# Optimization experiments

Measured on AMD Instinct MI355X. Metric: run time of the kernel, lower is better.

Reference implementation:

```python
import jax, jax.numpy as jnp
import numpy as np

B = 1024          # batch of positions
K = 64            # king squares
F = 640           # 64 squares * 10 piece types
C = 256           # accumulator channels


def setup_inputs() -> dict:
    key = jax.random.key(0)
    k1, k2, k3 = jax.random.split(key, 3)
    piece_positions = jax.random.randint(k1, (B, 64, 10), 0, 2).astype(jnp.bool_)
    king_positions = jax.random.randint(k2, (B, 2), 0, K, dtype=jnp.int32)
    input_weights = jax.random.normal(k3, (K, F + 1, C), dtype=jnp.float32)
    bias = jnp.zeros((C,), dtype=jnp.float32)
    return {
        "piece_positions": piece_positions,
        "king_positions": king_positions,
        "input_weights": input_weights,
        "bias": bias,
    }


def reference(piece_positions, king_positions, input_weights, bias):
    # Flatten the (64, 10) boolean piece plane into 640 HalfKP features.
    b = piece_positions.shape[0]
    p = piece_positions.reshape(b, F).astype(input_weights.dtype)          # (B, 640)
    # Gather each sample's white/black king weight slabs: (B, 2, 641, 256)
    Wg = jnp.take(input_weights, king_positions, axis=0)
    # Sparse-feature sum for both halves, contracted over feature dim and
    # summed over the two king perspectives in one einsum.
    halves = jnp.einsum("bf,bsfc->bc", p, Wg[:, :, :F, :])                 # (B, 256)
    extra = Wg[:, :, F, :].sum(axis=1)                                     # row 640 for each king
    return halves + extra + bias
```

## Files before the change

### kernel.cpp

```cpp
#include <hip/hip_runtime.h>
#include <hip/hip_bf16.h>


#define F_DIM 640
#define C_DIM 256
#define SLAB_STRIDE (641 * 256)
#define NKING 64
#define NBAND 7
#define WROWS 96
#define WPR 48
#define WSTR 260
#define LCAP 256
#define NC_MAX 64

#define WS_MASK_OFF 0
#define WS_PART_OFF 81920
#define WS_NEED (WS_PART_OFF + NBAND * 2 * 1024 * 256 * 4)

typedef float  f32x4  __attribute__((ext_vector_type(4)));
typedef short  bf16x8 __attribute__((ext_vector_type(8)));

__device__ __forceinline__ unsigned f2bf_pk(float a, float b) {
    union { float f; unsigned u; } x, y;
    x.f = a; y.f = b;
    const unsigned ra = (x.u + 0x7FFFu + ((x.u >> 16) & 1u)) >> 16;
    const unsigned rb = (y.u + 0x7FFFu + ((y.u >> 16) & 1u)) >> 16;
    return (ra & 0xFFFFu) | (rb << 16);
}

__device__ __forceinline__ bf16x8 mk_a8(unsigned m32, int g) {
    const unsigned by = (m32 >> (g * 8)) & 0xFFu;
    union { unsigned u[4]; bf16x8 v; } r;
    #pragma unroll
    for (int i = 0; i < 4; ++i)
        r.u[i] = (((by >> (2 * i)) & 1u) ? 0x3F80u : 0u) |
                 (((by >> (2 * i + 1)) & 1u) ? 0x3F800000u : 0u);
    return r.v;
}

__global__ __launch_bounds__(256)
void pack_masks(const int* __restrict__ pieces,
                unsigned long long* __restrict__ mask,
                int nwords)
{
    const int gw = blockIdx.x * 4 + (threadIdx.x >> 6);
    const int lane = threadIdx.x & 63;
    if (gw >= nwords) return;
    const int v = pieces[(size_t)gw * 64 + lane];
    const unsigned long long m = __ballot(v != 0);
    if (lane == 0) mask[gw] = m;
}

__global__ __launch_bounds__(512, 4)
void halfkp_kband(const float* __restrict__ W,
                  const unsigned long long* __restrict__ mask,
                  const int* __restrict__ kings,
                  float* __restrict__ partial,
                  int nent)
{
    const int k  = blockIdx.x;
    const int bd = blockIdx.y;
    const int t  = threadIdx.x;
    const int wv = t >> 6, lane = t & 63;
    const int mt = wv & 1;
    const int cg = wv >> 1;
    const int li = lane & 15, g = lane >> 4;

    __shared__ unsigned s_W[WPR * WSTR];
    __shared__ int s_ent[LCAP];
    __shared__ int s_cb[NC_MAX + 1];
    __shared__ unsigned s_m32[64][3];
    __shared__ int s_nk;

    const int r0 = bd * WROWS;
    const float* __restrict__ Wk = W + (size_t)k * SLAB_STRIDE;
    float4 ve[6], vo[6];
    #pragma unroll
    for (int it = 0; it < 6; ++it) {
        const int task = t + (it << 9);
        const int pr = task >> 6, c4 = task & 63;
        const int fe = min(r0 + 2 * pr, F_DIM);
        const int fo = min(r0 + 2 * pr + 1, F_DIM);
        ve[it] = *(const float4*)&Wk[(size_t)fe * C_DIM + c4 * 4];
        vo[it] = *(const float4*)&Wk[(size_t)fo * C_DIM + c4 * 4];
    }

    {
        const int NC = nent >> 6;
        const int nit = NC >> 3;
        unsigned long long mm[8];
        #pragma unroll
        for (int it = 0; it < 8; ++it) {
            if (it < nit) {
                const int c = wv + (it << 3);
                const int kk = kings[(c << 6) + lane];
                mm[it] = __ballot(kk == k);
                if (lane == 0) s_cb[c] = (int)__popcll(mm[it]);
            }
        }
        __syncthreads();
        if (t == 0) {
            int s = 0;
            for (int c = 0; c < NC; ++c) { const int v = s_cb[c]; s_cb[c] = s; s += v; }
            s_nk = min(s, LCAP);
        }
        __syncthreads();
        const unsigned long long lt = (1ull << lane) - 1ull;
        #pragma unroll
        for (int it = 0; it < 8; ++it) {
            if (it < nit) {
                const int c = wv + (it << 3);
                if ((mm[it] >> lane) & 1ull) {
                    const int pos = s_cb[c] + (int)__popcll(mm[it] & lt);
                    if (pos < LCAP) s_ent[pos] = (c << 6) + lane;
                }
            }
        }
    }
    __syncthreads();
    const int n_k = s_nk;

    {
        const int ncc0 = min(n_k, 64);
        for (int idx = t; idx < 64 * 3; idx += 512) {
            const int row = idx & 63, ksl = idx >> 6;
            const int ksg = bd * 3 + ksl;
            const int id = (row < ncc0) ? s_ent[row] : -1;
            unsigned v = 0;
            if (id >= 0) {
                if (ksg < 20) {
                    const unsigned long long mw = mask[(size_t)(id >> 1) * 10 + (ksg >> 1)];
                    v = (unsigned)(mw >> ((ksg & 1) * 32));
                } else {
                    v = 1u;
                }
            }
            s_m32[row][ksl] = v;
        }
    }

    #pragma unroll
    for (int it = 0; it < 6; ++it) {
        const int task = t + (it << 9);
        const int pr = task >> 6, c4 = task & 63;
        union { unsigned u[4]; f32x4 v; } pk;
        pk.u[0] = f2bf_pk(ve[it].x, vo[it].x);
        pk.u[1] = f2bf_pk(ve[it].y, vo[it].y);
        pk.u[2] = f2bf_pk(ve[it].z, vo[it].z);
        pk.u[3] = f2bf_pk(ve[it].w, vo[it].w);
        *(f32x4*)&s_W[pr * WSTR + c4 * 4] = pk.v;
    }
    __syncthreads();

    for (int mb = 0; mb < n_k; mb += 64) {
        const int ncc = min(n_k - mb, 64);

        if (mb > 0) {
            __syncthreads();
            for (int idx = t; idx < 64 * 3; idx += 512) {
                const int row = idx & 63, ksl = idx >> 6;
                const int ksg = bd * 3 + ksl;
                const int id = (row < ncc) ? s_ent[mb + row] : -1;
                unsigned v = 0;
                if (id >= 0) {
                    if (ksg < 20) {
                        const unsigned long long mw = mask[(size_t)(id >> 1) * 10 + (ksg >> 1)];
                        v = (unsigned)(mw >> ((ksg & 1) * 32));
                    } else {
                        v = 1u;
                    }
                }
                s_m32[row][ksl] = v;
            }
            __syncthreads();
        }

        #pragma unroll
        for (int tb = 0; tb < 4; tb += 2) {
            const int tile = tb + mt;
            if (tile * 16 < ncc) {
                f32x4 acc[4];
                #pragma unroll
                for (int nt = 0; nt < 4; ++nt) acc[nt] = (f32x4){0.f, 0.f, 0.f, 0.f};
                const unsigned* mrow = s_m32[tile * 16 + li];
                #pragma unroll
                for (int ksl = 0; ksl < 3; ++ksl) {
                    const bf16x8 af = mk_a8(mrow[ksl], g);
                    #pragma unroll
                    for (int nt = 0; nt < 4; ++nt) {
                        const unsigned* bp =
                            &s_W[(ksl * 16 + g * 4) * WSTR + cg * 64 + nt * 16 + li];
                        union { unsigned u[4]; bf16x8 v; } bb;
                        bb.u[0] = bp[0];
                        bb.u[1] = bp[WSTR];
                        bb.u[2] = bp[2 * WSTR];
                        bb.u[3] = bp[3 * WSTR];
                        acc[nt] = __builtin_amdgcn_mfma_f32_16x16x32_bf16(af, bb.v, acc[nt], 0, 0, 0);
                    }
                }
                #pragma unroll
                for (int i = 0; i < 4; ++i) {
                    const int r = tile * 16 + 4 * g + i;
                    if (r < ncc) {
                        const int id = s_ent[mb + r];
                        float* dst = &partial[(((size_t)(bd * 2 + (id & 1))) * 1024
                                              + (id >> 1)) * C_DIM + cg * 64];
                        #pragma unroll
                        for (int nt = 0; nt < 4; ++nt)
                            dst[nt * 16 + li] = acc[nt][i];
                    }
                }
            }
        }
    }
}

__global__ __launch_bounds__(256)
void finalize(const float* __restrict__ partial,
              const float* __restrict__ bias,
              float* __restrict__ out)
{
    const int i = blockIdx.x * 256 + threadIdx.x;
    float4 s = ((const float4*)bias)[i & 63];
    #pragma unroll
    for (int sl = 0; sl < NBAND * 2; ++sl) {
        const float4 p = ((const float4*)partial)[(size_t)sl * 1024 * 64 + i];
        s.x += p.x; s.y += p.y; s.z += p.z; s.w += p.w;
    }
    ((float4*)out)[i] = s;
}

__global__ __launch_bounds__(256)
void halfkp_fallback(const int* __restrict__ pieces, const int* __restrict__ kings,
                     const float* __restrict__ W, const float* __restrict__ bias,
                     float* __restrict__ out)
{
    const int b = blockIdx.x;
    const int c = threadIdx.x;
    const int lane = c & 63;
    const int k0 = kings[2 * b + 0];
    const int k1 = kings[2 * b + 1];
    const float* W0 = W + (size_t)k0 * SLAB_STRIDE + c;
    const float* W1 = W + (size_t)k1 * SLAB_STRIDE + c;
    float acc = bias[c] + W0[640 * 256] + W1[640 * 256];
    const int* pi = pieces + (size_t)b * F_DIM;
    #pragma unroll
    for (int ch = 0; ch < 10; ++ch) {
        int v = pi[ch * 64 + lane];
        unsigned long long m = __ballot(v != 0);
        const float* b0 = W0 + ch * 64 * 256;
        const float* b1 = W1 + ch * 64 * 256;
        while (m) {
            const int f = __builtin_ctzll(m);
            m &= m - 1;
            acc += b0[f * 256] + b1[f * 256];
        }
    }
    out[(size_t)b * C_DIM + c] = acc;
}

extern "C" void kernel_launch(void* const* d_in, const int* in_sizes, int n_in,
                              void* d_out, int out_size, void* d_ws, size_t ws_size,
                              hipStream_t stream) {
    const int* pieces = (const int*)d_in[0];
    const int* kings  = (const int*)d_in[1];
    const float* W    = (const float*)d_in[2];
    const float* bias = (const float*)d_in[3];
    float* out        = (float*)d_out;

    const int B = in_sizes[1] / 2;
    const int nent = 2 * B;
    const int nwords = B * 10;

    if (ws_size < (size_t)WS_NEED) {
        halfkp_fallback<<<dim3(B), dim3(C_DIM), 0, stream>>>(pieces, kings, W, bias, out);
        return;
    }

    unsigned long long* mask = (unsigned long long*)((char*)d_ws + WS_MASK_OFF);
    float* part = (float*)((char*)d_ws + WS_PART_OFF);

    pack_masks<<<dim3((nwords + 3) / 4), dim3(256), 0, stream>>>(pieces, mask, nwords);
    halfkp_kband<<<dim3(NKING, NBAND), dim3(512), 0, stream>>>(W, mask, kings, part, nent);
    finalize<<<dim3(B * 64 / 256), dim3(256), 0, stream>>>(part, bias, out);
}
```

Baseline: 27.87 us.

## Stage fp32 weight slabs via direct global-to-LDS loads with per-chunk bf16 conversion

Replaces the register-staged weight load, which converted to packed bf16 before writing LDS, with global_load_lds DMA of raw fp32 rows into a swizzled 32-row LDS buffer. The 96-row band is processed in three 32-row chunks, with a sync and restage between each, and bf16 packing is done at read time with v_cvt_pk_bf16_f32. This removes the register round-trip and shrinks LDS use, which could raise occupancy. The cost is extra barriers and serialised load-compute per chunk, plus conversion work repeated for every tile. For later mb iterations the weights are reloaded because the chunk buffer is overwritten.

```diff
diff --git a/kernel.cpp b/kernel.cpp
--- a/kernel.cpp
+++ b/kernel.cpp
@@ -7,9 +7,6 @@
 #define SLAB_STRIDE (641 * 256)
 #define NKING 64
 #define NBAND 7
-#define WROWS 96
-#define WPR 48
-#define WSTR 260
 #define LCAP 256
 #define NC_MAX 64
 
@@ -20,12 +17,10 @@
 typedef float  f32x4  __attribute__((ext_vector_type(4)));
 typedef short  bf16x8 __attribute__((ext_vector_type(8)));
 
-__device__ __forceinline__ unsigned f2bf_pk(float a, float b) {
-    union { float f; unsigned u; } x, y;
-    x.f = a; y.f = b;
-    const unsigned ra = (x.u + 0x7FFFu + ((x.u >> 16) & 1u)) >> 16;
-    const unsigned rb = (y.u + 0x7FFFu + ((y.u >> 16) & 1u)) >> 16;
-    return (ra & 0xFFFFu) | (rb << 16);
+__device__ __forceinline__ void gl_lds16(const float* g, unsigned* l) {
+    __builtin_amdgcn_global_load_lds(
+        (const __attribute__((address_space(1))) void*)g,
+        (__attribute__((address_space(3))) void*)l, 16, 0, 0);
 }
 
 __device__ __forceinline__ bf16x8 mk_a8(unsigned m32, int g) {
@@ -52,11 +47,11 @@
 }
 
 __global__ __launch_bounds__(512, 4)
-void halfkp_kband(const float* __restrict__ W,
-                  const unsigned long long* __restrict__ mask,
-                  const int* __restrict__ kings,
-                  float* __restrict__ partial,
-                  int nent)
+void halfkp_dma(const float* __restrict__ W,
+                const unsigned long long* __restrict__ mask,
+                const int* __restrict__ kings,
+                float* __restrict__ partial,
+                int nent)
 {
     const int k  = blockIdx.x;
     const int bd = blockIdx.y;
@@ -66,24 +61,27 @@
     const int cg = wv >> 1;
     const int li = lane & 15, g = lane >> 4;
 
-    __shared__ unsigned s_W[WPR * WSTR];
+    __shared__ unsigned s_Wf[32 * 256];
     __shared__ int s_ent[LCAP];
     __shared__ int s_cb[NC_MAX + 1];
     __shared__ unsigned s_m32[64][3];
     __shared__ int s_nk;
 
-    const int r0 = bd * WROWS;
     const float* __restrict__ Wk = W + (size_t)k * SLAB_STRIDE;
-    float4 ve[6], vo[6];
-    #pragma unroll
-    for (int it = 0; it < 6; ++it) {
-        const int task = t + (it << 9);
-        const int pr = task >> 6, c4 = task & 63;
-        const int fe = min(r0 + 2 * pr, F_DIM);
-        const int fo = min(r0 + 2 * pr + 1, F_DIM);
-        ve[it] = *(const float4*)&Wk[(size_t)fe * C_DIM + c4 * 4];
-        vo[it] = *(const float4*)&Wk[(size_t)fo * C_DIM + c4 * 4];
-    }
+
+    #define STAGE(ws_)                                                        \
+        {                                                                     \
+            _Pragma("unroll")                                                 \
+            for (int q = 0; q < 4; ++q) {                                     \
+                const int wr = wv * 4 + q;                                    \
+                const int frow = min(bd * 96 + (ws_) * 32 + wr, F_DIM);       \
+                const int lsw = lane ^ (((wr >> 3) & 3) << 2);                \
+                gl_lds16(Wk + (size_t)frow * C_DIM + lsw * 4,                 \
+                         &s_Wf[wr * 256]);                                    \
+            }                                                                 \
+        }
+
+    STAGE(0)
 
     {
         const int NC = nent >> 6;
@@ -138,19 +136,6 @@
             s_m32[row][ksl] = v;
         }
     }
-
-    #pragma unroll
-    for (int it = 0; it < 6; ++it) {
-        const int task = t + (it << 9);
-        const int pr = task >> 6, c4 = task & 63;
-        union { unsigned u[4]; f32x4 v; } pk;
-        pk.u[0] = f2bf_pk(ve[it].x, vo[it].x);
-        pk.u[1] = f2bf_pk(ve[it].y, vo[it].y);
-        pk.u[2] = f2bf_pk(ve[it].z, vo[it].z);
-        pk.u[3] = f2bf_pk(ve[it].w, vo[it].w);
-        *(f32x4*)&s_W[pr * WSTR + c4 * 4] = pk.v;
-    }
-    __syncthreads();
 
     for (int mb = 0; mb < n_k; mb += 64) {
         const int ncc = min(n_k - mb, 64);
@@ -172,32 +157,52 @@
                 }
                 s_m32[row][ksl] = v;
             }
-            __syncthreads();
-        }
-
-        #pragma unroll
-        for (int tb = 0; tb < 4; tb += 2) {
-            const int tile = tb + mt;
-            if (tile * 16 < ncc) {
-                f32x4 acc[4];
-                #pragma unroll
-                for (int nt = 0; nt < 4; ++nt) acc[nt] = (f32x4){0.f, 0.f, 0.f, 0.f};
-                const unsigned* mrow = s_m32[tile * 16 + li];
-                #pragma unroll
-                for (int ksl = 0; ksl < 3; ++ksl) {
-                    const bf16x8 af = mk_a8(mrow[ksl], g);
+            STAGE(0)
+        }
+        __syncthreads();
+
+        f32x4 acc[2][4];
+        #pragma unroll
+        for (int a = 0; a < 2; ++a)
+            #pragma unroll
+            for (int nt = 0; nt < 4; ++nt) acc[a][nt] = (f32x4){0.f, 0.f, 0.f, 0.f};
+
+        #pragma unroll
+        for (int ws = 0; ws < 3; ++ws) {
+            if (ws > 0) {
+                __syncthreads();
+                STAGE(ws)
+                __syncthreads();
+            }
+            #pragma unroll
+            for (int tb = 0; tb < 2; ++tb) {
+                const int tile = tb * 2 + mt;
+                if (tile * 16 < ncc) {
+                    const bf16x8 af = mk_a8(s_m32[tile * 16 + li][ws], g);
                     #pragma unroll
                     for (int nt = 0; nt < 4; ++nt) {
-                        const unsigned* bp =
-                            &s_W[(ksl * 16 + g * 4) * WSTR + cg * 64 + nt * 16 + li];
+                        const int col = cg * 64 + nt * 16 + li;
+                        const int colsw = col ^ (g << 4);
                         union { unsigned u[4]; bf16x8 v; } bb;
-                        bb.u[0] = bp[0];
-                        bb.u[1] = bp[WSTR];
-                        bb.u[2] = bp[2 * WSTR];
-                        bb.u[3] = bp[3 * WSTR];
-                        acc[nt] = __builtin_amdgcn_mfma_f32_16x16x32_bf16(af, bb.v, acc[nt], 0, 0, 0);
+                        #pragma unroll
+                        for (int jj = 0; jj < 4; ++jj) {
+                            const int rr = g * 8 + 2 * jj;
+                            const float lo = __uint_as_float(s_Wf[rr * 256 + colsw]);
+                            const float hi = __uint_as_float(s_Wf[(rr + 1) * 256 + colsw]);
+                            asm("v_cvt_pk_bf16_f32 %0, %1, %2"
+                                : "=v"(bb.u[jj]) : "v"(lo), "v"(hi));
+                        }
+                        acc[tb][nt] = __builtin_amdgcn_mfma_f32_16x16x32_bf16(
+                            af, bb.v, acc[tb][nt], 0, 0, 0);
                     }
                 }
+            }
+        }
+
+        #pragma unroll
+        for (int tb = 0; tb < 2; ++tb) {
+            const int tile = tb * 2 + mt;
+            if (tile * 16 < ncc) {
                 #pragma unroll
                 for (int i = 0; i < 4; ++i) {
                     const int r = tile * 16 + 4 * g + i;
@@ -207,12 +212,13 @@
                                               + (id >> 1)) * C_DIM + cg * 64];
                         #pragma unroll
                         for (int nt = 0; nt < 4; ++nt)
-                            dst[nt * 16 + li] = acc[nt][i];
+                            dst[nt * 16 + li] = acc[tb][nt][i];
                     }
                 }
             }
         }
     }
+    #undef STAGE
 }
 
 __global__ __launch_bounds__(256)
@@ -281,6 +287,6 @@
     float* part = (float*)((char*)d_ws + WS_PART_OFF);
 
     pack_masks<<<dim3((nwords + 3) / 4), dim3(256), 0, stream>>>(pieces, mask, nwords);
-    halfkp_kband<<<dim3(NKING, NBAND), dim3(512), 0, stream>>>(W, mask, kings, part, nent);
+    halfkp_dma<<<dim3(NKING, NBAND), dim3(512), 0, stream>>>(W, mask, kings, part, nent);
     finalize<<<dim3(B * 64 / 256), dim3(256), 0, stream>>>(part, bias, out);
 }
```

Result: faster. 26.72 us (-4.1%).
